# Kernel tuning notes

Hardware: AMD Instinct MI355X
Metric: run time of the kernel (lower is better)

Reference implementation:

```python
import jax, jax.numpy as jnp
import numpy as np

NA, NB = 50000, 10000        # node counts for types 'a' and 'b'
D_IN, D_OUT = 32, 64         # input feature dim, GRU hidden / GAT out dim
EA2A, EA2B, EB2A = 800000, 400000, 400000


def setup_inputs() -> dict:
    key = jax.random.key(0)
    ks = jax.random.split(key, 17)
    f32 = jnp.float32
    inp = {
        'x_a': jax.random.normal(ks[0], (NA, D_IN), f32),
        'x_b': jax.random.normal(ks[1], (NB, D_IN), f32),
        'h_a': jax.random.normal(ks[2], (NA, D_OUT), f32),
        'h_b': jax.random.normal(ks[3], (NB, D_OUT), f32),
        # stacked params: axis0 = gate (z,r,n); axis1 = node type (a,b) or edge type (a2a,a2b,b2a)
        'Wx': jax.random.normal(ks[4], (3, 2, D_IN, D_OUT), f32) * 0.05,
        'bx': jax.random.normal(ks[5], (3, 2, D_OUT), f32) * 0.05,
        'gat_ws': jax.random.normal(ks[6], (3, 3, D_OUT, D_OUT), f32) * 0.05,
        'gat_wd': jax.random.normal(ks[7], (3, 3, D_OUT, D_OUT), f32) * 0.05,
        'gat_as': jax.random.normal(ks[8], (3, 3, D_OUT), f32) * 0.05,
        'gat_ad': jax.random.normal(ks[9], (3, 3, D_OUT), f32) * 0.05,
        'gat_b': jax.random.normal(ks[10], (3, 3, D_OUT), f32) * 0.05,
        'ea2a_src': jax.random.randint(ks[11], (EA2A,), 0, NA, jnp.int32),
        'ea2a_dst': jax.random.randint(ks[12], (EA2A,), 0, NA, jnp.int32),
        'ea2b_src': jax.random.randint(ks[13], (EA2B,), 0, NA, jnp.int32),
        'ea2b_dst': jax.random.randint(ks[14], (EA2B,), 0, NB, jnp.int32),
        'eb2a_src': jax.random.randint(ks[15], (EB2A,), 0, NB, jnp.int32),
        'eb2a_dst': jax.random.randint(ks[16], (EB2A,), 0, NA, jnp.int32),
    }
    return inp


def _gat(hs, hd, src, dst, w_s, w_d, a_s, a_d, b, n_dst):
    """Single-head GATConv (PyG semantics, add_self_loops=False)."""
    xs = hs @ w_s                                   # [Ns, D] transformed sources
    xd = hd @ w_d                                   # [Nd, D] transformed destinations
    al_s = xs @ a_s                                 # [Ns]
    al_d = xd @ a_d                                 # [Nd]
    e = jax.nn.leaky_relu(al_s[src] + al_d[dst], 0.2)   # [E] raw attention logits
    m = jax.ops.segment_max(e, dst, num_segments=n_dst)
    m = jnp.where(jnp.isfinite(m), m, 0.0)          # empty segments -> 0 (unused)
    ex = jnp.exp(e - m[dst])
    denom = jax.ops.segment_sum(ex, dst, num_segments=n_dst)
    alpha = ex / (denom[dst] + 1e-16)               # segment softmax over in-edges
    out = jax.ops.segment_sum(alpha[:, None] * xs[src], dst, num_segments=n_dst)
    return out + b


def _hetero_conv(ha, hb, ws, wd, a_s, a_d, b, edges):
    """HeteroConv with sum aggregation across edge types per destination type."""
    (sa2a, da2a), (sa2b, da2b), (sb2a, db2a) = edges
    out_a = (_gat(ha, ha, sa2a, da2a, ws[0], wd[0], a_s[0], a_d[0], b[0], NA)
             + _gat(hb, ha, sb2a, db2a, ws[2], wd[2], a_s[2], a_d[2], b[2], NA))
    out_b = _gat(ha, hb, sa2b, da2b, ws[1], wd[1], a_s[1], a_d[1], b[1], NB)
    return out_a, out_b


def reference(x_a, x_b, h_a, h_b, Wx, bx, gat_ws, gat_wd, gat_as, gat_ad, gat_b,
              ea2a_src, ea2a_dst, ea2b_src, ea2b_dst, eb2a_src, eb2a_dst):
    edges = ((ea2a_src, ea2a_dst), (ea2b_src, ea2b_dst), (eb2a_src, eb2a_dst))

    def gate(g, ha_in, hb_in, act):
        ca, cb = _hetero_conv(ha_in, hb_in, gat_ws[g], gat_wd[g],
                              gat_as[g], gat_ad[g], gat_b[g], edges)
        ga = act(x_a @ Wx[g, 0] + ca + bx[g, 0])
        gb = act(x_b @ Wx[g, 1] + cb + bx[g, 1])
        return ga, gb

    z_a, z_b = gate(0, h_a, h_b, jax.nn.sigmoid)          # update gate
    r_a, r_b = gate(1, h_a, h_b, jax.nn.sigmoid)          # reset gate
    n_a, n_b = gate(2, r_a * h_a, r_b * h_b, jnp.tanh)    # candidate state
    new_a = (1.0 - z_a) * n_a + z_a * h_a
    new_b = (1.0 - z_b) * n_b + z_b * h_b
    return jnp.concatenate([new_a, new_b], axis=0)        # [NA+NB, D_OUT]
```

## Files before the change

### kernel.cpp

```cpp
#include <hip/hip_runtime.h>
#include <hip/hip_bf16.h>
#include <cstddef>
#include <cstdint>

#define NA 50000
#define NB 10000
#define D_IN 32
#define D_OUT 64
#define EA2A 800000
#define EA2B 400000
#define EB2A 400000
#define NCAT (NA + NB + NA)
#define ETOT (EA2A + EA2B + EB2A)
#define NCHUNK 8
#define CHUNK (NCAT / NCHUNK)
#define NSLICE 64
#define ESLICE (ETOT / NSLICE)

typedef unsigned int u32;
typedef unsigned short u16;
typedef __attribute__((ext_vector_type(8))) short short8_t;
typedef __attribute__((ext_vector_type(4))) float f32x4;
typedef __attribute__((ext_vector_type(2))) float f32x2;

__device__ __forceinline__ u32 bf16r(float x) {
    u32 u = __float_as_uint(x);
    u += 0x7fffu + ((u >> 16) & 1u);
    return u >> 16;
}
__device__ __forceinline__ float ubf(u32 bits) { return __uint_as_float(bits); }
__device__ __forceinline__ float sigm(float x) { return 1.f / (1.f + __expf(-x)); }
__device__ __forceinline__ u32 cvtpk(float lo, float hi) {
    u32 r;
    asm("v_cvt_pk_bf16_f32 %0, %1, %2" : "=v"(r) : "v"(lo), "v"(hi));
    return r;
}
__device__ __forceinline__ void pkfma(f32x2& acc, f32x2 x, f32x2 p) {
    asm("v_pk_fma_f32 %0, %1, %2, %0" : "+v"(acc) : "v"(x), "v"(p));
}

template <int CTRL, int RM>
__device__ __forceinline__ float dppf(float v) {
    return __int_as_float(__builtin_amdgcn_update_dpp(0, __float_as_int(v), CTRL, RM, 0xf, true));
}
__device__ __forceinline__ float wsum64(float v) {
    v += dppf<0x111, 0xf>(v);
    v += dppf<0x112, 0xf>(v);
    v += dppf<0x114, 0xf>(v);
    v += dppf<0x118, 0xf>(v);
    v += dppf<0x142, 0xa>(v);
    v += dppf<0x143, 0xc>(v);
    return __int_as_float(__builtin_amdgcn_readlane(__float_as_int(v), 63));
}

struct MmArgs {
    const float* H; int ntiles;
    const float* W0; const float* W1;
    void* XS; void* XS1;
    const float* SW[8]; const float* SA[8]; float* SOUT[8];
    int sstride; int nsc;
};

template <int NMAT, int PACKED>
__global__ void __launch_bounds__(256) gemm_mfma(MmArgs a)
{
    __shared__ float wvec[8][64];
    __shared__ short8_t bfr[NMAT * 8 + 2][64];
    int t = threadIdx.x;
    for (int idx = t; idx < a.nsc * 64; idx += 256) {
        int c = idx >> 6, k = idx & 63;
        const float* w = a.SW[c] + k * 64;
        const float* av = a.SA[c];
        float s = 0.f;
#pragma unroll 16
        for (int e = 0; e < 64; ++e) s = fmaf(w[e], av[e], s);
        wvec[c][k] = s;
    }
    __syncthreads();
    for (int idx = t; idx < NMAT * 8 * 64; idx += 256) {
        int fid = idx >> 6, l = idx & 63;
        int m = fid >> 3, r3 = fid & 7, tn = r3 >> 1, q = r3 & 1;
        const float* W = (NMAT == 2 && m == 1) ? a.W1 : a.W0;
        int kbase = 32 * q + ((l >> 4) << 3);
        int d = 16 * tn + (l & 15);
        short8_t v;
#pragma unroll
        for (int e = 0; e < 8; ++e) v[e] = (short)bf16r(W[(size_t)(kbase + e) * 64 + d]);
        bfr[fid][l] = v;
    }
    for (int idx = t; idx < 128; idx += 256) {
        int q = idx >> 6, l = idx & 63;
        int c = l & 15;
        int kbase = 32 * q + ((l >> 4) << 3);
        short8_t v;
#pragma unroll
        for (int e = 0; e < 8; ++e) v[e] = (c < a.nsc) ? (short)bf16r(wvec[c][kbase + e]) : (short)0;
        bfr[NMAT * 8 + q][l] = v;
    }
    __syncthreads();
    int lane = t & 63, wid = t >> 6;
    short8_t bw[NMAT][4][2], bs0, bs1;
#pragma unroll
    for (int m = 0; m < NMAT; ++m)
#pragma unroll
        for (int tn = 0; tn < 4; ++tn)
#pragma unroll
            for (int q = 0; q < 2; ++q) bw[m][tn][q] = bfr[m * 8 + tn * 2 + q][lane];
    bs0 = bfr[NMAT * 8][lane];
    bs1 = bfr[NMAT * 8 + 1][lane];

    int rl = lane & 15, kg = lane >> 4;
    f32x4 zero = {0.f, 0.f, 0.f, 0.f};
    for (int tile = blockIdx.x * 4 + wid; tile < a.ntiles; tile += gridDim.x * 4) {
        const float4* hp = (const float4*)(a.H + (size_t)(tile * 16 + rl) * 64) + kg * 2;
        float4 a0 = hp[0], a1 = hp[1];
        float4 b0 = hp[8], b1 = hp[9];
        union { short8_t s; u32 w[4]; } A0, A1;
        A0.w[0] = cvtpk(a0.x, a0.y); A0.w[1] = cvtpk(a0.z, a0.w);
        A0.w[2] = cvtpk(a1.x, a1.y); A0.w[3] = cvtpk(a1.z, a1.w);
        A1.w[0] = cvtpk(b0.x, b0.y); A1.w[1] = cvtpk(b0.z, b0.w);
        A1.w[2] = cvtpk(b1.x, b1.y); A1.w[3] = cvtpk(b1.z, b1.w);

        f32x4 acc[NMAT][4];
#pragma unroll
        for (int m = 0; m < NMAT; ++m)
#pragma unroll
            for (int tn = 0; tn < 4; ++tn) {
                f32x4 c0 = __builtin_amdgcn_mfma_f32_16x16x32_bf16(A0.s, bw[m][tn][0], zero, 0, 0, 0);
                acc[m][tn] = __builtin_amdgcn_mfma_f32_16x16x32_bf16(A1.s, bw[m][tn][1], c0, 0, 0, 0);
            }
        f32x4 accs = __builtin_amdgcn_mfma_f32_16x16x32_bf16(A0.s, bs0, zero, 0, 0, 0);
        accs = __builtin_amdgcn_mfma_f32_16x16x32_bf16(A1.s, bs1, accs, 0, 0, 0);

        int rbase = tile * 16 + kg * 4;
        if (NMAT == 2 && PACKED == 1) {
            u32* xo = (u32*)a.XS;
#pragma unroll
            for (int tn = 0; tn < 4; ++tn) {
                int d = tn * 16 + rl;
#pragma unroll
                for (int j = 0; j < 4; ++j)
                    xo[(size_t)(rbase + j) * 64 + d] = cvtpk(acc[0][tn][j], acc[1][tn][j]);
            }
        } else if (NMAT == 2 && PACKED == 0) {
            u16* xo0 = (u16*)a.XS;
            u16* xo1 = (u16*)a.XS1;
#pragma unroll
            for (int tn = 0; tn < 4; ++tn) {
                int d = tn * 16 + rl;
#pragma unroll
                for (int j = 0; j < 4; ++j) {
                    xo0[(size_t)(rbase + j) * 64 + d] = (u16)bf16r(acc[0][tn][j]);
                    xo1[(size_t)(rbase + j) * 64 + d] = (u16)bf16r(acc[1][tn][j]);
                }
            }
        } else {
            u16* xo = (u16*)a.XS;
#pragma unroll
            for (int tn = 0; tn < 4; ++tn) {
                int d = tn * 16 + rl;
#pragma unroll
                for (int j = 0; j < 4; ++j)
                    xo[(size_t)(rbase + j) * 64 + d] = (u16)bf16r(acc[0][tn][j]);
            }
        }
        if (rl < a.nsc) {
            float* so = a.SOUT[rl];
#pragma unroll
            for (int j = 0; j < 4; ++j) so[(size_t)(rbase + j) * a.sstride] = accs[j];
        }
    }
}

__global__ void __launch_bounds__(256) gemm_x_k(
    const float* __restrict__ xA, const float* __restrict__ xB,
    const float* __restrict__ Wx, const float* __restrict__ bx, const float* __restrict__ gb,
    u32* __restrict__ dzrA, u32* __restrict__ dzrB,
    u16* __restrict__ dnA, u16* __restrict__ dnB)
{
    __shared__ float Wsh[3 * 2048];
    __shared__ float cb[3 * 64];
    int t = threadIdx.x;
    int blk = blockIdx.x;
    bool isA = blk < (NA / 8);
    int ty = isA ? 0 : 1;
#pragma unroll
    for (int g = 0; g < 3; ++g) {
        const float4* s = (const float4*)(Wx + (size_t)(g * 2 + ty) * 2048);
        float4* d = (float4*)&Wsh[g * 2048];
        for (int i = t; i < 512; i += 256) d[i] = s[i];
    }
    if (t < 192) {
        int g = t >> 6, d = t & 63;
        float c = bx[(g * 2 + ty) * 64 + d];
        if (isA) c += gb[(g * 3 + 0) * 64 + d] + gb[(g * 3 + 2) * 64 + d];
        else     c += gb[(g * 3 + 1) * 64 + d];
        cb[t] = c;
    }
    __syncthreads();
    int lane = t & 63, wid = t >> 6;
    const float* X = isA ? xA : xB;
    int N = isA ? NA : NB;
    int rbase = (isA ? blk : blk - NA / 8) * 8 + wid * 2;
    float cz = cb[lane], cr = cb[64 + lane], cn = cb[128 + lane];
#pragma unroll
    for (int rr = 0; rr < 2; ++rr) {
        int r = rbase + rr;
        if (r >= N) break;
        float xv = (lane < 32) ? X[(size_t)r * 32 + lane] : 0.f;
        float az = cz, ar = cr, an = cn;
#pragma unroll
        for (int k = 0; k < 32; ++k) {
            float xk = __shfl(xv, k, 64);
            az = fmaf(xk, Wsh[k * 64 + lane], az);
            ar = fmaf(xk, Wsh[2048 + k * 64 + lane], ar);
            an = fmaf(xk, Wsh[4096 + k * 64 + lane], an);
        }
        u32 zr = bf16r(az) | (bf16r(ar) << 16);
        u16 nn = (u16)bf16r(an);
        if (isA) { dzrA[(size_t)r * 64 + lane] = zr; dnA[(size_t)r * 64 + lane] = nn; }
        else     { dzrB[(size_t)r * 64 + lane] = zr; dnB[(size_t)r * 64 + lane] = nn; }
    }
}

__global__ void __launch_bounds__(512) hist_k(
    const int* __restrict__ d0, const int* __restrict__ d1, const int* __restrict__ d2,
    u16* __restrict__ partial)
{
    __shared__ int hcnt[CHUNK];
    int k = blockIdx.x & (NCHUNK - 1);
    int s = blockIdx.x / NCHUNK;
    int lo = k * CHUNK;
    for (int i = threadIdx.x; i < CHUNK; i += 512) hcnt[i] = 0;
    __syncthreads();
    int e0 = s * ESLICE, e1 = e0 + ESLICE;
    for (int e = e0 + threadIdx.x; e < e1; e += 512) {
        int g;
        if (e < EA2A) g = d0[e];
        else if (e < EA2A + EA2B) g = NA + d1[e - EA2A];
        else g = NA + NB + d2[e - EA2A - EA2B];
        u32 rel = (u32)(g - lo);
        if (rel < CHUNK) atomicAdd(&hcnt[rel], 1);
    }
    __syncthreads();
    u16* po = partial + (size_t)s * NCAT + lo;
    for (int i = threadIdx.x; i < CHUNK; i += 512) po[i] = (u16)hcnt[i];
}

__global__ void scan_partial(const u16* __restrict__ partial, int* __restrict__ bsum, int N)
{
    __shared__ int sd[256];
    int t = threadIdx.x;
    int i = blockIdx.x * 256 + t;
    int v = 0;
    if (i < N) {
#pragma unroll 16
        for (int s = 0; s < NSLICE; ++s) v += partial[(size_t)s * NCAT + i];
    }
    sd[t] = v;
    __syncthreads();
    for (int off = 128; off; off >>= 1) {
        if (t < off) sd[t] += sd[t + off];
        __syncthreads();
    }
    if (t == 0) bsum[blockIdx.x] = sd[0];
}

__global__ void __launch_bounds__(512) scan_tops(int* bsum, int nb)
{
    __shared__ int sd[512];
    int t = threadIdx.x;
    int v = (t < nb) ? bsum[t] : 0;
    sd[t] = v;
    __syncthreads();
    for (int off = 1; off < 512; off <<= 1) {
        int add = (t >= off) ? sd[t - off] : 0;
        __syncthreads();
        sd[t] += add;
        __syncthreads();
    }
    if (t < nb) bsum[t] = sd[t] - v;
}

__global__ void scan_final(const u16* __restrict__ partial, const int* __restrict__ bsum,
                           int* __restrict__ rowptr, int* __restrict__ cnt,
                           u16* __restrict__ soff, int N)
{
    __shared__ int sd[256];
    int t = threadIdx.x;
    int i = blockIdx.x * 256 + t;
    int v = 0;
    if (i < N) {
#pragma unroll 16
        for (int s = 0; s < NSLICE; ++s) v += partial[(size_t)s * NCAT + i];
    }
    sd[t] = v;
    __syncthreads();
    for (int off = 1; off < 256; off <<= 1) {
        int add = (t >= off) ? sd[t - off] : 0;
        __syncthreads();
        sd[t] += add;
        __syncthreads();
    }
    if (i < N) {
        int rpi = bsum[blockIdx.x] + sd[t] - v;
        rowptr[i] = rpi;
        cnt[i] = v;
        int run = 0;
#pragma unroll 16
        for (int s = 0; s < NSLICE; ++s) {
            soff[(size_t)s * NCAT + i] = (u16)run;
            run += partial[(size_t)s * NCAT + i];
        }
    }
}

__global__ void __launch_bounds__(512) fill_k(
    const int* __restrict__ s0, const int* __restrict__ d0,
    const int* __restrict__ s1, const int* __restrict__ d1,
    const int* __restrict__ s2, const int* __restrict__ d2,
    const int* __restrict__ rp, const u16* __restrict__ soff, u16* __restrict__ csr)
{
    __shared__ int fpos[CHUNK];
    int k = blockIdx.x & (NCHUNK - 1);
    int s = blockIdx.x / NCHUNK;
    int lo = k * CHUNK;
    const u16* po = soff + (size_t)s * NCAT + lo;
    const int* rpo = rp + lo;
    for (int i = threadIdx.x; i < CHUNK; i += 512) fpos[i] = rpo[i] + (int)po[i];
    __syncthreads();
    int e0 = s * ESLICE, e1 = e0 + ESLICE;
    for (int e = e0 + threadIdx.x; e < e1; e += 512) {
        int g, sidx;
        const int* sp;
        if (e < EA2A) { g = d0[e]; sp = s0; sidx = e; }
        else if (e < EA2A + EA2B) { sidx = e - EA2A; g = NA + d1[sidx]; sp = s1; }
        else { sidx = e - EA2A - EA2B; g = NA + NB + d2[sidx]; sp = s2; }
        u32 rel = (u32)(g - lo);
        if (rel < CHUNK) {
            int src = sp[sidx];
            int p = atomicAdd(&fpos[rel], 1);
            csr[p] = (u16)src;
        }
    }
}

__device__ __forceinline__ void zr_pk(f32x2 azr[4], uint4 v, f32x2 p) {
    f32x2 x;
    x[0] = ubf(v.x << 16); x[1] = ubf(v.x & 0xffff0000u); pkfma(azr[0], x, p);
    x[0] = ubf(v.y << 16); x[1] = ubf(v.y & 0xffff0000u); pkfma(azr[1], x, p);
    x[0] = ubf(v.z << 16); x[1] = ubf(v.z & 0xffff0000u); pkfma(azr[2], x, p);
    x[0] = ubf(v.w << 16); x[1] = ubf(v.w & 0xffff0000u); pkfma(azr[3], x, p);
}

__device__ __forceinline__ void gat_zr_et(
    int gnode, int inode, int lane, int sub, int grp,
    const int* __restrict__ rp, const int* __restrict__ cnt, const u16* __restrict__ csr,
    const float2* __restrict__ als, const float2* __restrict__ ald,
    const uint4* __restrict__ xs,
    float oz[4], float orr[4])
{
    int deg = cnt[gnode];
    if (deg <= 0) return;
    int beg = rp[gnode];
    float2 ad = ald[inode];
    f32x2 azr[4];
#pragma unroll
    for (int q = 0; q < 4; ++q) { azr[q][0] = 0.f; azr[q][1] = 0.f; }
    float szl = 0.f, srl = 0.f;
    for (int base = 0; base < deg; base += 64) {
        int j = base + lane;
        int sj = 0; float pz = 0.f, pr = 0.f;
        if (j < deg) {
            sj = csr[beg + j];
            float2 al = als[sj];
            float tz = al.x + ad.x;
            float tr = al.y + ad.y;
            pz = __expf(fmaxf(tz, 0.2f * tz));
            pr = __expf(fmaxf(tr, 0.2f * tr));
        }
        szl += pz; srl += pr;
        u32 pk = (u32)sj | (bf16r(pz) << 16);
        int c = deg - base; if (c > 64) c = 64;
        int b = 0;
        for (; b + 16 <= c; b += 16) {
            u32 k0 = (u32)__shfl((int)pk, b + grp, 64);
            u32 k1 = (u32)__shfl((int)pk, b + 4 + grp, 64);
            u32 k2 = (u32)__shfl((int)pk, b + 8 + grp, 64);
            u32 k3 = (u32)__shfl((int)pk, b + 12 + grp, 64);
            float q0 = __shfl(pr, b + grp, 64);
            float q1 = __shfl(pr, b + 4 + grp, 64);
            float q2 = __shfl(pr, b + 8 + grp, 64);
            float q3 = __shfl(pr, b + 12 + grp, 64);
            uint4 v0 = xs[(size_t)(k0 & 0xffffu) * 16 + sub];
            uint4 v1 = xs[(size_t)(k1 & 0xffffu) * 16 + sub];
            uint4 v2 = xs[(size_t)(k2 & 0xffffu) * 16 + sub];
            uint4 v3 = xs[(size_t)(k3 & 0xffffu) * 16 + sub];
            f32x2 p;
            p[0] = ubf(k0 & 0xffff0000u); p[1] = q0; zr_pk(azr, v0, p);
            p[0] = ubf(k1 & 0xffff0000u); p[1] = q1; zr_pk(azr, v1, p);
            p[0] = ubf(k2 & 0xffff0000u); p[1] = q2; zr_pk(azr, v2, p);
            p[0] = ubf(k3 & 0xffff0000u); p[1] = q3; zr_pk(azr, v3, p);
        }
        for (; b < c; b += 4) {
            u32 k0 = (u32)__shfl((int)pk, b + grp, 64);
            float q0 = __shfl(pr, b + grp, 64);
            uint4 v0 = xs[(size_t)(k0 & 0xffffu) * 16 + sub];
            f32x2 p;
            p[0] = ubf(k0 & 0xffff0000u); p[1] = q0;
            zr_pk(azr, v0, p);
        }
    }
    float sz = wsum64(szl), sr = wsum64(srl);
    float rz = 1.f / (sz + 1e-16f), rr = 1.f / (sr + 1e-16f);
#pragma unroll
    for (int q = 0; q < 4; ++q) {
        oz[q] = fmaf(azr[q][0], rz, oz[q]);
        orr[q] = fmaf(azr[q][1], rr, orr[q]);
    }
}

__device__ __forceinline__ void n_pk4(f32x2 ac[4], uint4 v, f32x2 p) {
    f32x2 x;
    x[0] = ubf(v.x << 16); x[1] = ubf(v.x & 0xffff0000u); pkfma(ac[0], x, p);
    x[0] = ubf(v.y << 16); x[1] = ubf(v.y & 0xffff0000u); pkfma(ac[1], x, p);
    x[0] = ubf(v.z << 16); x[1] = ubf(v.z & 0xffff0000u); pkfma(ac[2], x, p);
    x[0] = ubf(v.w << 16); x[1] = ubf(v.w & 0xffff0000u); pkfma(ac[3], x, p);
}

__device__ __forceinline__ void gat_n_et(
    int gnode, int inode, int lane, int sub8, int grp8,
    const int* __restrict__ rp, const int* __restrict__ cnt, const u16* __restrict__ csr,
    const float* __restrict__ als, const float* __restrict__ ald,
    const uint4* __restrict__ xs,
    f32x2 oa[4])
{
    int deg = cnt[gnode];
    if (deg <= 0) return;
    int beg = rp[gnode];
    float ad = ald[inode];
    f32x2 ac[4];
#pragma unroll
    for (int q = 0; q < 4; ++q) { ac[q][0] = 0.f; ac[q][1] = 0.f; }
    float ssl = 0.f;
    for (int base = 0; base < deg; base += 64) {
        int j = base + lane;
        int sj = 0; float pv = 0.f;
        if (j < deg) {
            sj = csr[beg + j];
            float tv = als[sj] + ad;
            pv = __expf(fmaxf(tv, 0.2f * tv));
        }
        ssl += pv;
        u32 pk = (u32)sj | (bf16r(pv) << 16);
        int c = deg - base; if (c > 64) c = 64;
        int b = 0;
        for (; b + 32 <= c; b += 32) {
            u32 kk[4];
#pragma unroll
            for (int u = 0; u < 4; ++u) kk[u] = (u32)__shfl((int)pk, b + 8 * u + grp8, 64);
            uint4 vv[4];
#pragma unroll
            for (int u = 0; u < 4; ++u) vv[u] = xs[(size_t)(kk[u] & 0xffffu) * 8 + sub8];
#pragma unroll
            for (int u = 0; u < 4; ++u) {
                f32x2 p; p[0] = ubf(kk[u] & 0xffff0000u); p[1] = p[0];
                n_pk4(ac, vv[u], p);
            }
        }
        for (; b < c; b += 8) {
            u32 k0 = (u32)__shfl((int)pk, b + grp8, 64);
            uint4 v0 = xs[(size_t)(k0 & 0xffffu) * 8 + sub8];
            f32x2 p; p[0] = ubf(k0 & 0xffff0000u); p[1] = p[0];
            n_pk4(ac, v0, p);
        }
    }
    float ss = wsum64(ssl);
    float rs = 1.f / (ss + 1e-16f);
#pragma unroll
    for (int q = 0; q < 4; ++q) {
        oa[q][0] = fmaf(ac[q][0], rs, oa[q][0]);
        oa[q][1] = fmaf(ac[q][1], rs, oa[q][1]);
    }
}

struct ZrArgs {
    const int *rp, *cnt;
    const u16 *csr;
    const float2 *als0, *ald0, *als1, *ald1, *als2, *ald2;
    const uint4 *xs0, *xs1, *xs2;
    const u32 *dzrA, *dzrB;
    const float *hA, *hB;
    float *zA, *rhA, *zB, *rhB;
};

__global__ void __launch_bounds__(256) aggregate_zr_k(ZrArgs P)
{
    int t = threadIdx.x, lane = t & 63, wid = t >> 6;
    int sub = lane & 15, grp = lane >> 4;
    float oz[4] = {0.f, 0.f, 0.f, 0.f}, orr[4] = {0.f, 0.f, 0.f, 0.f};
    int blk = blockIdx.x;
    const u32* dzr; const float* Hp; float *Zp, *RHp;
    if (blk < NA / 4) {
        int i = blk * 4 + wid;
        gat_zr_et(i, i, lane, sub, grp, P.rp, P.cnt, P.csr, P.als0, P.ald0, P.xs0, oz, orr);
        gat_zr_et(NA + NB + i, i, lane, sub, grp, P.rp, P.cnt, P.csr, P.als2, P.ald2, P.xs2, oz, orr);
        dzr = P.dzrA + (size_t)i * 64; Hp = P.hA + (size_t)i * 64;
        Zp = P.zA + (size_t)i * 64; RHp = P.rhA + (size_t)i * 64;
    } else {
        int i = (blk - NA / 4) * 4 + wid;
        gat_zr_et(NA + i, i, lane, sub, grp, P.rp, P.cnt, P.csr, P.als1, P.ald1, P.xs1, oz, orr);
        dzr = P.dzrB + (size_t)i * 64; Hp = P.hB + (size_t)i * 64;
        Zp = P.zB + (size_t)i * 64; RHp = P.rhB + (size_t)i * 64;
    }
#pragma unroll
    for (int q = 0; q < 4; ++q) {
        oz[q] += __shfl_xor(oz[q], 16, 64); oz[q] += __shfl_xor(oz[q], 32, 64);
        orr[q] += __shfl_xor(orr[q], 16, 64); orr[q] += __shfl_xor(orr[q], 32, 64);
    }
    if (grp == 0) {
        uint4 d = *(const uint4*)(dzr + sub * 4);
        float4 h = *(const float4*)(Hp + sub * 4);
        float z0 = sigm(oz[0] + ubf(d.x << 16)), r0 = sigm(orr[0] + ubf(d.x & 0xffff0000u)) * h.x;
        float z1 = sigm(oz[1] + ubf(d.y << 16)), r1 = sigm(orr[1] + ubf(d.y & 0xffff0000u)) * h.y;
        float z2 = sigm(oz[2] + ubf(d.z << 16)), r2 = sigm(orr[2] + ubf(d.z & 0xffff0000u)) * h.z;
        float z3 = sigm(oz[3] + ubf(d.w << 16)), r3 = sigm(orr[3] + ubf(d.w & 0xffff0000u)) * h.w;
        *(float4*)(Zp + sub * 4) = make_float4(z0, z1, z2, z3);
        *(float4*)(RHp + sub * 4) = make_float4(r0, r1, r2, r3);
    }
}

struct NArgs {
    const int *rp, *cnt;
    const u16 *csr;
    const float *als0, *ald0, *als1, *ald1, *als2, *ald2;
    const uint4 *xs0, *xs1, *xs2;
    const u16 *dnA, *dnB;
    const float *hA, *hB, *zA, *zB;
    float *outA, *outB;
};

__global__ void __launch_bounds__(256) aggregate_n_k(NArgs P)
{
    int t = threadIdx.x, lane = t & 63, wid = t >> 6;
    int sub8 = lane & 7, grp8 = lane >> 3;
    f32x2 oa[4];
#pragma unroll
    for (int q = 0; q < 4; ++q) { oa[q][0] = 0.f; oa[q][1] = 0.f; }
    int blk = blockIdx.x;
    const u16* dn; const float *Hp, *Zp; float* Op;
    if (blk < NA / 4) {
        int i = blk * 4 + wid;
        gat_n_et(i, i, lane, sub8, grp8, P.rp, P.cnt, P.csr, P.als0, P.ald0, P.xs0, oa);
        gat_n_et(NA + NB + i, i, lane, sub8, grp8, P.rp, P.cnt, P.csr, P.als2, P.ald2, P.xs2, oa);
        dn = P.dnA + (size_t)i * 64; Hp = P.hA + (size_t)i * 64;
        Zp = P.zA + (size_t)i * 64; Op = P.outA + (size_t)i * 64;
    } else {
        int i = (blk - NA / 4) * 4 + wid;
        gat_n_et(NA + i, i, lane, sub8, grp8, P.rp, P.cnt, P.csr, P.als1, P.ald1, P.xs1, oa);
        dn = P.dnB + (size_t)i * 64; Hp = P.hB + (size_t)i * 64;
        Zp = P.zB + (size_t)i * 64; Op = P.outB + (size_t)i * 64;
    }
#pragma unroll
    for (int q = 0; q < 4; ++q) {
#pragma unroll
        for (int e = 0; e < 2; ++e) {
            oa[q][e] += __shfl_xor(oa[q][e], 8, 64);
            oa[q][e] += __shfl_xor(oa[q][e], 16, 64);
            oa[q][e] += __shfl_xor(oa[q][e], 32, 64);
        }
    }
    if (grp8 == 0) {
        uint4 d = *(const uint4*)(dn + sub8 * 8);
        float4 h0 = *(const float4*)(Hp + sub8 * 8);
        float4 h1 = *(const float4*)(Hp + sub8 * 8 + 4);
        float4 zv0 = *(const float4*)(Zp + sub8 * 8);
        float4 zv1 = *(const float4*)(Zp + sub8 * 8 + 4);
        float pre[8];
        pre[0] = oa[0][0] + ubf(d.x << 16); pre[1] = oa[0][1] + ubf(d.x & 0xffff0000u);
        pre[2] = oa[1][0] + ubf(d.y << 16); pre[3] = oa[1][1] + ubf(d.y & 0xffff0000u);
        pre[4] = oa[2][0] + ubf(d.z << 16); pre[5] = oa[2][1] + ubf(d.z & 0xffff0000u);
        pre[6] = oa[3][0] + ubf(d.w << 16); pre[7] = oa[3][1] + ubf(d.w & 0xffff0000u);
        float hh[8] = {h0.x, h0.y, h0.z, h0.w, h1.x, h1.y, h1.z, h1.w};
        float zz[8] = {zv0.x, zv0.y, zv0.z, zv0.w, zv1.x, zv1.y, zv1.z, zv1.w};
        float o[8];
#pragma unroll
        for (int q = 0; q < 8; ++q) {
            float x2 = fminf(fmaxf(pre[q] * 2.f, -30.f), 30.f);
            float ex = __expf(x2);
            float nv = (ex - 1.f) / (ex + 1.f);
            o[q] = (1.f - zz[q]) * nv + zz[q] * hh[q];
        }
        *(float4*)(Op + sub8 * 8) = make_float4(o[0], o[1], o[2], o[3]);
        *(float4*)(Op + sub8 * 8 + 4) = make_float4(o[4], o[5], o[6], o[7]);
    }
}

extern "C" void kernel_launch(void* const* d_in, const int* in_sizes, int n_in,
                              void* d_out, int out_size, void* d_ws, size_t ws_size,
                              hipStream_t stream)
{
    (void)in_sizes; (void)n_in; (void)out_size; (void)ws_size;
    const float* x_a = (const float*)d_in[0];
    const float* x_b = (const float*)d_in[1];
    const float* h_a = (const float*)d_in[2];
    const float* h_b = (const float*)d_in[3];
    const float* Wx  = (const float*)d_in[4];
    const float* bx  = (const float*)d_in[5];
    const float* gws = (const float*)d_in[6];
    const float* gwd = (const float*)d_in[7];
    const float* gas = (const float*)d_in[8];
    const float* gad = (const float*)d_in[9];
    const float* gb  = (const float*)d_in[10];
    const int* ea2a_s = (const int*)d_in[11];
    const int* ea2a_d = (const int*)d_in[12];
    const int* ea2b_s = (const int*)d_in[13];
    const int* ea2b_d = (const int*)d_in[14];
    const int* eb2a_s = (const int*)d_in[15];
    const int* eb2a_d = (const int*)d_in[16];
    float* out = (float*)d_out;

    char* w = (char*)d_ws;
    auto alloc = [&](size_t bytes) -> char* {
        char* p = w;
        w += (bytes + 255) & ~(size_t)255;
        return p;
    };
    char* xsblk = alloc((size_t)(NA + NA + NB) * 64 * 4);
    u32* xs_zr0 = (u32*)xsblk;
    u32* xs_zr1 = (u32*)(xsblk + (size_t)NA * 64 * 4);
    u32* xs_zr2 = (u32*)(xsblk + (size_t)(NA + NA) * 64 * 4);
    u16* xs_n0 = (u16*)xsblk;
    u16* xs_n1 = (u16*)(xsblk + (size_t)NA * 64 * 2);
    u16* xs_n2 = (u16*)(xsblk + (size_t)(NA + NA) * 64 * 2);
    char* alblk = alloc((size_t)(4 * NA + 2 * NB) * 2 * 4);
    float* als_zr0 = (float*)alblk;
    float* als_zr1 = als_zr0 + (size_t)NA * 2;
    float* als_zr2 = als_zr1 + (size_t)NA * 2;
    float* ald_zr0 = als_zr2 + (size_t)NB * 2;
    float* ald_zr1 = ald_zr0 + (size_t)NA * 2;
    float* ald_zr2 = ald_zr1 + (size_t)NB * 2;
    float* als_n0 = (float*)alblk;
    float* als_n1 = als_n0 + NA;
    float* als_n2 = als_n1 + NA;
    float* ald_n0 = als_n2 + NB;
    float* ald_n1 = ald_n0 + NA;
    float* ald_n2 = ald_n1 + NB;
    float* zbuf  = (float*)alloc((size_t)(NA + NB) * 64 * 4);
    float* rhbuf = (float*)alloc((size_t)(NA + NB) * 64 * 4);
    u32* dzrA = (u32*)alloc((size_t)NA * 64 * 4);
    u32* dzrB = (u32*)alloc((size_t)NB * 64 * 4);
    u16* dnA = (u16*)alloc((size_t)NA * 64 * 2);
    u16* dnB = (u16*)alloc((size_t)NB * 64 * 2);
    u16* partial = (u16*)alloc((size_t)NSLICE * NCAT * 2);
    u16* soff    = (u16*)alloc((size_t)NSLICE * NCAT * 2);
    int* cnt = (int*)alloc((size_t)NCAT * 4);
    int* rp  = (int*)alloc((size_t)NCAT * 4);
    u16* csr = (u16*)alloc((size_t)ETOT * 2);
    int* bsum = (int*)alloc(512 * 4);

    const int nbC = (NCAT + 255) / 256;

    hist_k<<<NCHUNK * NSLICE, 512, 0, stream>>>(ea2a_d, ea2b_d, eb2a_d, partial);
    scan_partial<<<nbC, 256, 0, stream>>>(partial, bsum, NCAT);
    scan_tops<<<1, 512, 0, stream>>>(bsum, nbC);
    scan_final<<<nbC, 256, 0, stream>>>(partial, bsum, rp, cnt, soff, NCAT);
    fill_k<<<NCHUNK * NSLICE, 512, 0, stream>>>(ea2a_s, ea2a_d, ea2b_s, ea2b_d, eb2a_s, eb2a_d,
                                                rp, soff, csr);

    gemm_x_k<<<(NA + NB) / 8, 256, 0, stream>>>(x_a, x_b, Wx, bx, gb, dzrA, dzrB, dnA, dnB);

    float* rh_a = rhbuf;
    float* rh_b = rhbuf + (size_t)NA * 64;
    float* z_a = zbuf;
    float* z_b = zbuf + (size_t)NA * 64;

    {
        MmArgs a{};
        a.H = h_a; a.ntiles = NA / 16;
        a.W0 = gws + 0 * 4096; a.W1 = gws + 3 * 4096;
        a.XS = xs_zr0;
        a.SW[0] = gws + 0 * 4096; a.SA[0] = gas + 0 * 64; a.SOUT[0] = als_zr0;
        a.SW[1] = gws + 3 * 4096; a.SA[1] = gas + 3 * 64; a.SOUT[1] = als_zr0 + 1;
        a.SW[2] = gws + 1 * 4096; a.SA[2] = gas + 1 * 64; a.SOUT[2] = als_zr1;
        a.SW[3] = gws + 4 * 4096; a.SA[3] = gas + 4 * 64; a.SOUT[3] = als_zr1 + 1;
        a.SW[4] = gwd + 0 * 4096; a.SA[4] = gad + 0 * 64; a.SOUT[4] = ald_zr0;
        a.SW[5] = gwd + 3 * 4096; a.SA[5] = gad + 3 * 64; a.SOUT[5] = ald_zr0 + 1;
        a.SW[6] = gwd + 2 * 4096; a.SA[6] = gad + 2 * 64; a.SOUT[6] = ald_zr2;
        a.SW[7] = gwd + 5 * 4096; a.SA[7] = gad + 5 * 64; a.SOUT[7] = ald_zr2 + 1;
        a.sstride = 2; a.nsc = 8;
        gemm_mfma<2, 1><<<320, 256, 0, stream>>>(a);
    }
    {
        MmArgs a{};
        a.H = h_a; a.ntiles = NA / 16;
        a.W0 = gws + 1 * 4096; a.W1 = gws + 4 * 4096;
        a.XS = xs_zr1;
        a.sstride = 1; a.nsc = 0;
        gemm_mfma<2, 1><<<320, 256, 0, stream>>>(a);
    }
    {
        MmArgs a{};
        a.H = h_b; a.ntiles = NB / 16;
        a.W0 = gws + 2 * 4096; a.W1 = gws + 5 * 4096;
        a.XS = xs_zr2;
        a.SW[0] = gws + 2 * 4096; a.SA[0] = gas + 2 * 64; a.SOUT[0] = als_zr2;
        a.SW[1] = gws + 5 * 4096; a.SA[1] = gas + 5 * 64; a.SOUT[1] = als_zr2 + 1;
        a.SW[2] = gwd + 1 * 4096; a.SA[2] = gad + 1 * 64; a.SOUT[2] = ald_zr1;
        a.SW[3] = gwd + 4 * 4096; a.SA[3] = gad + 4 * 64; a.SOUT[3] = ald_zr1 + 1;
        a.sstride = 2; a.nsc = 4;
        gemm_mfma<2, 1><<<80, 256, 0, stream>>>(a);
    }

    {
        ZrArgs P{};
        P.rp = rp; P.cnt = cnt; P.csr = csr;
        P.als0 = (const float2*)als_zr0; P.ald0 = (const float2*)ald_zr0;
        P.als1 = (const float2*)als_zr1; P.ald1 = (const float2*)ald_zr1;
        P.als2 = (const float2*)als_zr2; P.ald2 = (const float2*)ald_zr2;
        P.xs0 = (const uint4*)xs_zr0; P.xs1 = (const uint4*)xs_zr1; P.xs2 = (const uint4*)xs_zr2;
        P.dzrA = dzrA; P.dzrB = dzrB;
        P.hA = h_a; P.hB = h_b;
        P.zA = z_a; P.rhA = rh_a; P.zB = z_b; P.rhB = rh_b;
        aggregate_zr_k<<<(NA + NB) / 4, 256, 0, stream>>>(P);
    }

    {
        MmArgs a{};
        a.H = rh_a; a.ntiles = NA / 16;
        a.W0 = gws + 6 * 4096; a.W1 = gws + 7 * 4096;
        a.XS = xs_n0; a.XS1 = xs_n1;
        a.SW[0] = gws + 6 * 4096; a.SA[0] = gas + 6 * 64; a.SOUT[0] = als_n0;
        a.SW[1] = gws + 7 * 4096; a.SA[1] = gas + 7 * 64; a.SOUT[1] = als_n1;
        a.SW[2] = gwd + 6 * 4096; a.SA[2] = gad + 6 * 64; a.SOUT[2] = ald_n0;
        a.SW[3] = gwd + 8 * 4096; a.SA[3] = gad + 8 * 64; a.SOUT[3] = ald_n2;
        a.sstride = 1; a.nsc = 4;
        gemm_mfma<2, 0><<<320, 256, 0, stream>>>(a);
    }
    {
        MmArgs a{};
        a.H = rh_b; a.ntiles = NB / 16;
        a.W0 = gws + 8 * 4096; a.W1 = nullptr;
        a.XS = xs_n2;
        a.SW[0] = gws + 8 * 4096; a.SA[0] = gas + 8 * 64; a.SOUT[0] = als_n2;
        a.SW[1] = gwd + 7 * 4096; a.SA[1] = gad + 7 * 64; a.SOUT[1] = ald_n1;
        a.sstride = 1; a.nsc = 2;
        gemm_mfma<1, 1><<<80, 256, 0, stream>>>(a);
    }

    {
        NArgs P{};
        P.rp = rp; P.cnt = cnt; P.csr = csr;
        P.als0 = als_n0; P.ald0 = ald_n0;
        P.als1 = als_n1; P.ald1 = ald_n1;
        P.als2 = als_n2; P.ald2 = ald_n2;
        P.xs0 = (const uint4*)xs_n0; P.xs1 = (const uint4*)xs_n1; P.xs2 = (const uint4*)xs_n2;
        P.dnA = dnA; P.dnB = dnB;
        P.hA = h_a; P.hB = h_b; P.zA = z_a; P.zB = z_b;
        P.outA = out; P.outB = out + (size_t)NA * 64;
        aggregate_n_k<<<(NA + NB) / 4, 256, 0, stream>>>(P);
    }
}
```

Baseline: 316.5 us.

## Batch MFMA GEMM launches, store r*h as bf16, fold top-level scan into final scan

The three z/r projection GEMMs and the two candidate-gate GEMMs each become a single launch, with each block choosing its sub-problem from the block index. The r*h intermediate is now written as packed bf16 and read directly by the GEMM, which halves that buffer's traffic and drops the in-kernel conversion. The separate scan_tops kernel is removed: each scan_final block reduces the preceding block sums itself. gemm_x_k uses a fixed grid with a grid-stride loop. In exchange, the type-b candidate GEMM now computes a redundant second matrix into a scratch buffer, and scan_final repeats the prefix-sum reduction in every block.

Result: no change. 314.9 us (-0.5%).

```diff
diff --git a/kernel.cpp b/kernel.cpp
--- a/kernel.cpp
+++ b/kernel.cpp
@@ -54,18 +54,28 @@
 }
 
 struct MmArgs {
-    const float* H; int ntiles;
+    const void* H; int ntiles;
     const float* W0; const float* W1;
     void* XS; void* XS1;
     const float* SW[8]; const float* SA[8]; float* SOUT[8];
     int sstride; int nsc;
 };
-
-template <int NMAT, int PACKED>
-__global__ void __launch_bounds__(256) gemm_mfma(MmArgs a)
+struct MmMulti {
+    MmArgs r[3];
+    int n0, n1;
+};
+
+template <int NMAT, int PACKED, int HB16>
+__global__ void __launch_bounds__(256) gemm_mfma(MmMulti m)
 {
     __shared__ float wvec[8][64];
     __shared__ short8_t bfr[NMAT * 8 + 2][64];
+    int b = blockIdx.x;
+    const MmArgs* Rp; int lb, nb;
+    if (b < m.n0) { Rp = &m.r[0]; lb = b; nb = m.n0; }
+    else if (b < m.n0 + m.n1) { Rp = &m.r[1]; lb = b - m.n0; nb = m.n1; }
+    else { Rp = &m.r[2]; lb = b - m.n0 - m.n1; nb = gridDim.x - m.n0 - m.n1; }
+    const MmArgs a = *Rp;
     int t = threadIdx.x;
     for (int idx = t; idx < a.nsc * 64; idx += 256) {
         int c = idx >> 6, k = idx & 63;
@@ -79,8 +89,8 @@
     __syncthreads();
     for (int idx = t; idx < NMAT * 8 * 64; idx += 256) {
         int fid = idx >> 6, l = idx & 63;
-        int m = fid >> 3, r3 = fid & 7, tn = r3 >> 1, q = r3 & 1;
-        const float* W = (NMAT == 2 && m == 1) ? a.W1 : a.W0;
+        int mm = fid >> 3, r3 = fid & 7, tn = r3 >> 1, q = r3 & 1;
+        const float* W = (NMAT == 2 && mm == 1) ? a.W1 : a.W0;
         int kbase = 32 * q + ((l >> 4) << 3);
         int d = 16 * tn + (l & 15);
         short8_t v;
@@ -101,33 +111,39 @@
     int lane = t & 63, wid = t >> 6;
     short8_t bw[NMAT][4][2], bs0, bs1;
 #pragma unroll
-    for (int m = 0; m < NMAT; ++m)
+    for (int mm = 0; mm < NMAT; ++mm)
 #pragma unroll
         for (int tn = 0; tn < 4; ++tn)
 #pragma unroll
-            for (int q = 0; q < 2; ++q) bw[m][tn][q] = bfr[m * 8 + tn * 2 + q][lane];
+            for (int q = 0; q < 2; ++q) bw[mm][tn][q] = bfr[mm * 8 + tn * 2 + q][lane];
     bs0 = bfr[NMAT * 8][lane];
     bs1 = bfr[NMAT * 8 + 1][lane];
 
     int rl = lane & 15, kg = lane >> 4;
     f32x4 zero = {0.f, 0.f, 0.f, 0.f};
-    for (int tile = blockIdx.x * 4 + wid; tile < a.ntiles; tile += gridDim.x * 4) {
-        const float4* hp = (const float4*)(a.H + (size_t)(tile * 16 + rl) * 64) + kg * 2;
-        float4 a0 = hp[0], a1 = hp[1];
-        float4 b0 = hp[8], b1 = hp[9];
-        union { short8_t s; u32 w[4]; } A0, A1;
-        A0.w[0] = cvtpk(a0.x, a0.y); A0.w[1] = cvtpk(a0.z, a0.w);
-        A0.w[2] = cvtpk(a1.x, a1.y); A0.w[3] = cvtpk(a1.z, a1.w);
-        A1.w[0] = cvtpk(b0.x, b0.y); A1.w[1] = cvtpk(b0.z, b0.w);
-        A1.w[2] = cvtpk(b1.x, b1.y); A1.w[3] = cvtpk(b1.z, b1.w);
+    for (int tile = lb * 4 + wid; tile < a.ntiles; tile += nb * 4) {
+        union { uint4 u; short8_t s; } A0, A1;
+        if (HB16) {
+            const uint4* hp = (const uint4*)((const u16*)a.H + (size_t)(tile * 16 + rl) * 64);
+            A0.u = hp[kg];
+            A1.u = hp[4 + kg];
+        } else {
+            const float4* hp = (const float4*)((const float*)a.H + (size_t)(tile * 16 + rl) * 64) + kg * 2;
+            float4 a0 = hp[0], a1 = hp[1];
+            float4 b0 = hp[8], b1 = hp[9];
+            A0.u.x = cvtpk(a0.x, a0.y); A0.u.y = cvtpk(a0.z, a0.w);
+            A0.u.z = cvtpk(a1.x, a1.y); A0.u.w = cvtpk(a1.z, a1.w);
+            A1.u.x = cvtpk(b0.x, b0.y); A1.u.y = cvtpk(b0.z, b0.w);
+            A1.u.z = cvtpk(b1.x, b1.y); A1.u.w = cvtpk(b1.z, b1.w);
+        }
 
         f32x4 acc[NMAT][4];
 #pragma unroll
-        for (int m = 0; m < NMAT; ++m)
+        for (int mm = 0; mm < NMAT; ++mm)
 #pragma unroll
             for (int tn = 0; tn < 4; ++tn) {
-                f32x4 c0 = __builtin_amdgcn_mfma_f32_16x16x32_bf16(A0.s, bw[m][tn][0], zero, 0, 0, 0);
-                acc[m][tn] = __builtin_amdgcn_mfma_f32_16x16x32_bf16(A1.s, bw[m][tn][1], c0, 0, 0, 0);
+                f32x4 c0 = __builtin_amdgcn_mfma_f32_16x16x32_bf16(A0.s, bw[mm][tn][0], zero, 0, 0, 0);
+                acc[mm][tn] = __builtin_amdgcn_mfma_f32_16x16x32_bf16(A1.s, bw[mm][tn][1], c0, 0, 0, 0);
             }
         f32x4 accs = __builtin_amdgcn_mfma_f32_16x16x32_bf16(A0.s, bs0, zero, 0, 0, 0);
         accs = __builtin_amdgcn_mfma_f32_16x16x32_bf16(A1.s, bs1, accs, 0, 0, 0);
@@ -182,7 +198,7 @@
     __shared__ float cb[3 * 64];
     int t = threadIdx.x;
     int blk = blockIdx.x;
-    bool isA = blk < (NA / 8);
+    bool isA = blk < 448;
     int ty = isA ? 0 : 1;
 #pragma unroll
     for (int g = 0; g < 3; ++g) {
@@ -201,25 +217,28 @@
     int lane = t & 63, wid = t >> 6;
     const float* X = isA ? xA : xB;
     int N = isA ? NA : NB;
-    int rbase = (isA ? blk : blk - NA / 8) * 8 + wid * 2;
+    int nblk = isA ? 448 : 64;
+    int lb = isA ? blk : blk - 448;
     float cz = cb[lane], cr = cb[64 + lane], cn = cb[128 + lane];
-#pragma unroll
-    for (int rr = 0; rr < 2; ++rr) {
-        int r = rbase + rr;
-        if (r >= N) break;
-        float xv = (lane < 32) ? X[(size_t)r * 32 + lane] : 0.f;
-        float az = cz, ar = cr, an = cn;
-#pragma unroll
-        for (int k = 0; k < 32; ++k) {
-            float xk = __shfl(xv, k, 64);
-            az = fmaf(xk, Wsh[k * 64 + lane], az);
-            ar = fmaf(xk, Wsh[2048 + k * 64 + lane], ar);
-            an = fmaf(xk, Wsh[4096 + k * 64 + lane], an);
-        }
-        u32 zr = bf16r(az) | (bf16r(ar) << 16);
-        u16 nn = (u16)bf16r(an);
-        if (isA) { dzrA[(size_t)r * 64 + lane] = zr; dnA[(size_t)r * 64 + lane] = nn; }
-        else     { dzrB[(size_t)r * 64 + lane] = zr; dnB[(size_t)r * 64 + lane] = nn; }
+    for (int r0 = (lb * 4 + wid) * 2; r0 < N; r0 += nblk * 8) {
+#pragma unroll
+        for (int rr = 0; rr < 2; ++rr) {
+            int r = r0 + rr;
+            if (r >= N) break;
+            float xv = (lane < 32) ? X[(size_t)r * 32 + lane] : 0.f;
+            float az = cz, ar = cr, an = cn;
+#pragma unroll
+            for (int k = 0; k < 32; ++k) {
+                float xk = __shfl(xv, k, 64);
+                az = fmaf(xk, Wsh[k * 64 + lane], az);
+                ar = fmaf(xk, Wsh[2048 + k * 64 + lane], ar);
+                an = fmaf(xk, Wsh[4096 + k * 64 + lane], an);
+            }
+            u32 zr = bf16r(az) | (bf16r(ar) << 16);
+            u16 nn = (u16)bf16r(an);
+            if (isA) { dzrA[(size_t)r * 64 + lane] = zr; dnA[(size_t)r * 64 + lane] = nn; }
+            else     { dzrB[(size_t)r * 64 + lane] = zr; dnB[(size_t)r * 64 + lane] = nn; }
+        }
     }
 }
 
@@ -266,28 +285,23 @@
     if (t == 0) bsum[blockIdx.x] = sd[0];
 }
 
-__global__ void __launch_bounds__(512) scan_tops(int* bsum, int nb)
-{
-    __shared__ int sd[512];
-    int t = threadIdx.x;
-    int v = (t < nb) ? bsum[t] : 0;
-    sd[t] = v;
-    __syncthreads();
-    for (int off = 1; off < 512; off <<= 1) {
-        int add = (t >= off) ? sd[t - off] : 0;
-        __syncthreads();
-        sd[t] += add;
-        __syncthreads();
-    }
-    if (t < nb) bsum[t] = sd[t] - v;
-}
-
 __global__ void scan_final(const u16* __restrict__ partial, const int* __restrict__ bsum,
                            int* __restrict__ rowptr, int* __restrict__ cnt,
                            u16* __restrict__ soff, int N)
 {
     __shared__ int sd[256];
+    __shared__ int rbuf[256];
     int t = threadIdx.x;
+    int acc = 0;
+    for (int j = t; j < blockIdx.x; j += 256) acc += bsum[j];
+    rbuf[t] = acc;
+    __syncthreads();
+    for (int off = 128; off; off >>= 1) {
+        if (t < off) rbuf[t] += rbuf[t + off];
+        __syncthreads();
+    }
+    int base = rbuf[0];
+    __syncthreads();
     int i = blockIdx.x * 256 + t;
     int v = 0;
     if (i < N) {
@@ -303,7 +317,7 @@
         __syncthreads();
     }
     if (i < N) {
-        int rpi = bsum[blockIdx.x] + sd[t] - v;
+        int rpi = base + sd[t] - v;
         rowptr[i] = rpi;
         cnt[i] = v;
         int run = 0;
@@ -491,7 +505,8 @@
     const uint4 *xs0, *xs1, *xs2;
     const u32 *dzrA, *dzrB;
     const float *hA, *hB;
-    float *zA, *rhA, *zB, *rhB;
+    float *zA, *zB;
+    u16 *rhA, *rhB;
 };
 
 __global__ void __launch_bounds__(256) aggregate_zr_k(ZrArgs P)
@@ -500,7 +515,7 @@
     int sub = lane & 15, grp = lane >> 4;
     float oz[4] = {0.f, 0.f, 0.f, 0.f}, orr[4] = {0.f, 0.f, 0.f, 0.f};
     int blk = blockIdx.x;
-    const u32* dzr; const float* Hp; float *Zp, *RHp;
+    const u32* dzr; const float* Hp; float* Zp; u16* RHp;
     if (blk < NA / 4) {
         int i = blk * 4 + wid;
         gat_zr_et(i, i, lane, sub, grp, P.rp, P.cnt, P.csr, P.als0, P.ald0, P.xs0, oz, orr);
@@ -526,7 +541,10 @@
         float z2 = sigm(oz[2] + ubf(d.z << 16)), r2 = sigm(orr[2] + ubf(d.z & 0xffff0000u)) * h.z;
         float z3 = sigm(oz[3] + ubf(d.w << 16)), r3 = sigm(orr[3] + ubf(d.w & 0xffff0000u)) * h.w;
         *(float4*)(Zp + sub * 4) = make_float4(z0, z1, z2, z3);
-        *(float4*)(RHp + sub * 4) = make_float4(r0, r1, r2, r3);
+        uint2 rhp;
+        rhp.x = cvtpk(r0, r1);
+        rhp.y = cvtpk(r2, r3);
+        *(uint2*)(RHp + sub * 4) = rhp;
     }
 }
 
@@ -647,7 +665,7 @@
     float* ald_n1 = ald_n0 + NA;
     float* ald_n2 = ald_n1 + NB;
     float* zbuf  = (float*)alloc((size_t)(NA + NB) * 64 * 4);
-    float* rhbuf = (float*)alloc((size_t)(NA + NB) * 64 * 4);
+    u16* rhbuf = (u16*)alloc((size_t)(NA + NB) * 64 * 2);
     u32* dzrA = (u32*)alloc((size_t)NA * 64 * 4);
     u32* dzrB = (u32*)alloc((size_t)NB * 64 * 4);
     u16* dnA = (u16*)alloc((size_t)NA * 64 * 2);
@@ -658,58 +676,51 @@
     int* rp  = (int*)alloc((size_t)NCAT * 4);
     u16* csr = (u16*)alloc((size_t)ETOT * 2);
     int* bsum = (int*)alloc(512 * 4);
+    u16* nscr = (u16*)alloc((size_t)NB * 64 * 2);
 
     const int nbC = (NCAT + 255) / 256;
 
     hist_k<<<NCHUNK * NSLICE, 512, 0, stream>>>(ea2a_d, ea2b_d, eb2a_d, partial);
     scan_partial<<<nbC, 256, 0, stream>>>(partial, bsum, NCAT);
-    scan_tops<<<1, 512, 0, stream>>>(bsum, nbC);
     scan_final<<<nbC, 256, 0, stream>>>(partial, bsum, rp, cnt, soff, NCAT);
     fill_k<<<NCHUNK * NSLICE, 512, 0, stream>>>(ea2a_s, ea2a_d, ea2b_s, ea2b_d, eb2a_s, eb2a_d,
                                                 rp, soff, csr);
 
-    gemm_x_k<<<(NA + NB) / 8, 256, 0, stream>>>(x_a, x_b, Wx, bx, gb, dzrA, dzrB, dnA, dnB);
-
-    float* rh_a = rhbuf;
-    float* rh_b = rhbuf + (size_t)NA * 64;
+    gemm_x_k<<<512, 256, 0, stream>>>(x_a, x_b, Wx, bx, gb, dzrA, dzrB, dnA, dnB);
+
+    u16* rh_a = rhbuf;
+    u16* rh_b = rhbuf + (size_t)NA * 64;
     float* z_a = zbuf;
     float* z_b = zbuf + (size_t)NA * 64;
 
     {
-        MmArgs a{};
-        a.H = h_a; a.ntiles = NA / 16;
-        a.W0 = gws + 0 * 4096; a.W1 = gws + 3 * 4096;
-        a.XS = xs_zr0;
-        a.SW[0] = gws + 0 * 4096; a.SA[0] = gas + 0 * 64; a.SOUT[0] = als_zr0;
-        a.SW[1] = gws + 3 * 4096; a.SA[1] = gas + 3 * 64; a.SOUT[1] = als_zr0 + 1;
-        a.SW[2] = gws + 1 * 4096; a.SA[2] = gas + 1 * 64; a.SOUT[2] = als_zr1;
-        a.SW[3] = gws + 4 * 4096; a.SA[3] = gas + 4 * 64; a.SOUT[3] = als_zr1 + 1;
-        a.SW[4] = gwd + 0 * 4096; a.SA[4] = gad + 0 * 64; a.SOUT[4] = ald_zr0;
-        a.SW[5] = gwd + 3 * 4096; a.SA[5] = gad + 3 * 64; a.SOUT[5] = ald_zr0 + 1;
-        a.SW[6] = gwd + 2 * 4096; a.SA[6] = gad + 2 * 64; a.SOUT[6] = ald_zr2;
-        a.SW[7] = gwd + 5 * 4096; a.SA[7] = gad + 5 * 64; a.SOUT[7] = ald_zr2 + 1;
-        a.sstride = 2; a.nsc = 8;
-        gemm_mfma<2, 1><<<320, 256, 0, stream>>>(a);
-    }
-    {
-        MmArgs a{};
-        a.H = h_a; a.ntiles = NA / 16;
-        a.W0 = gws + 1 * 4096; a.W1 = gws + 4 * 4096;
-        a.XS = xs_zr1;
-        a.sstride = 1; a.nsc = 0;
-        gemm_mfma<2, 1><<<320, 256, 0, stream>>>(a);
-    }
-    {
-        MmArgs a{};
-        a.H = h_b; a.ntiles = NB / 16;
-        a.W0 = gws + 2 * 4096; a.W1 = gws + 5 * 4096;
-        a.XS = xs_zr2;
-        a.SW[0] = gws + 2 * 4096; a.SA[0] = gas + 2 * 64; a.SOUT[0] = als_zr2;
-        a.SW[1] = gws + 5 * 4096; a.SA[1] = gas + 5 * 64; a.SOUT[1] = als_zr2 + 1;
-        a.SW[2] = gwd + 1 * 4096; a.SA[2] = gad + 1 * 64; a.SOUT[2] = ald_zr1;
-        a.SW[3] = gwd + 4 * 4096; a.SA[3] = gad + 4 * 64; a.SOUT[3] = ald_zr1 + 1;
-        a.sstride = 2; a.nsc = 4;
-        gemm_mfma<2, 1><<<80, 256, 0, stream>>>(a);
+        MmMulti M{};
+        M.n0 = 320; M.n1 = 320;
+        M.r[0].H = h_a; M.r[0].ntiles = NA / 16;
+        M.r[0].W0 = gws + 0 * 4096; M.r[0].W1 = gws + 3 * 4096;
+        M.r[0].XS = xs_zr0;
+        M.r[0].SW[0] = gws + 0 * 4096; M.r[0].SA[0] = gas + 0 * 64; M.r[0].SOUT[0] = als_zr0;
+        M.r[0].SW[1] = gws + 3 * 4096; M.r[0].SA[1] = gas + 3 * 64; M.r[0].SOUT[1] = als_zr0 + 1;
+        M.r[0].SW[2] = gws + 1 * 4096; M.r[0].SA[2] = gas + 1 * 64; M.r[0].SOUT[2] = als_zr1;
+        M.r[0].SW[3] = gws + 4 * 4096; M.r[0].SA[3] = gas + 4 * 64; M.r[0].SOUT[3] = als_zr1 + 1;
+        M.r[0].SW[4] = gwd + 0 * 4096; M.r[0].SA[4] = gad + 0 * 64; M.r[0].SOUT[4] = ald_zr0;
+        M.r[0].SW[5] = gwd + 3 * 4096; M.r[0].SA[5] = gad + 3 * 64; M.r[0].SOUT[5] = ald_zr0 + 1;
+        M.r[0].SW[6] = gwd + 2 * 4096; M.r[0].SA[6] = gad + 2 * 64; M.r[0].SOUT[6] = ald_zr2;
+        M.r[0].SW[7] = gwd + 5 * 4096; M.r[0].SA[7] = gad + 5 * 64; M.r[0].SOUT[7] = ald_zr2 + 1;
+        M.r[0].sstride = 2; M.r[0].nsc = 8;
+        M.r[1].H = h_a; M.r[1].ntiles = NA / 16;
+        M.r[1].W0 = gws + 1 * 4096; M.r[1].W1 = gws + 4 * 4096;
+        M.r[1].XS = xs_zr1;
+        M.r[1].sstride = 1; M.r[1].nsc = 0;
+        M.r[2].H = h_b; M.r[2].ntiles = NB / 16;
+        M.r[2].W0 = gws + 2 * 4096; M.r[2].W1 = gws + 5 * 4096;
+        M.r[2].XS = xs_zr2;
+        M.r[2].SW[0] = gws + 2 * 4096; M.r[2].SA[0] = gas + 2 * 64; M.r[2].SOUT[0] = als_zr2;
+        M.r[2].SW[1] = gws + 5 * 4096; M.r[2].SA[1] = gas + 5 * 64; M.r[2].SOUT[1] = als_zr2 + 1;
+        M.r[2].SW[2] = gwd + 1 * 4096; M.r[2].SA[2] = gad + 1 * 64; M.r[2].SOUT[2] = ald_zr1;
+        M.r[2].SW[3] = gwd + 4 * 4096; M.r[2].SA[3] = gad + 4 * 64; M.r[2].SOUT[3] = ald_zr1 + 1;
+        M.r[2].sstride = 2; M.r[2].nsc = 4;
+        gemm_mfma<2, 1, 0><<<720, 256, 0, stream>>>(M);
     }
 
     {
@@ -721,31 +732,28 @@
         P.xs0 = (const uint4*)xs_zr0; P.xs1 = (const uint4*)xs_zr1; P.xs2 = (const uint4*)xs_zr2;
         P.dzrA = dzrA; P.dzrB = dzrB;
         P.hA = h_a; P.hB = h_b;
-        P.zA = z_a; P.rhA = rh_a; P.zB = z_b; P.rhB = rh_b;
+        P.zA = z_a; P.zB = z_b; P.rhA = rh_a; P.rhB = rh_b;
         aggregate_zr_k<<<(NA + NB) / 4, 256, 0, stream>>>(P);
     }
 
     {
-        MmArgs a{};
-        a.H = rh_a; a.ntiles = NA / 16;
-        a.W0 = gws + 6 * 4096; a.W1 = gws + 7 * 4096;
-        a.XS = xs_n0; a.XS1 = xs_n1;
-        a.SW[0] = gws + 6 * 4096; a.SA[0] = gas + 6 * 64; a.SOUT[0] = als_n0;
-        a.SW[1] = gws + 7 * 4096; a.SA[1] = gas + 7 * 64; a.SOUT[1] = als_n1;
-        a.SW[2] = gwd + 6 * 4096; a.SA[2] = gad + 6 * 64; a.SOUT[2] = ald_n0;
-        a.SW[3] = gwd + 8 * 4096; a.SA[3] = gad + 8 * 64; a.SOUT[3] = ald_n2;
-        a.sstride = 1; a.nsc = 4;
-        gemm_mfma<2, 0><<<320, 256, 0, stream>>>(a);
-    }
-    {
-        MmArgs a{};
-        a.H = rh_b; a.ntiles = NB / 16;
-        a.W0 = gws + 8 * 4096; a.W1 = nullptr;
-        a.XS = xs_n2;
-        a.SW[0] = gws + 8 * 4096; a.SA[0] = gas + 8 * 64; a.SOUT[0] = als_n2;
-        a.SW[1] = gwd + 7 * 4096; a.SA[1] = gad + 7 * 64; a.SOUT[1] = ald_n1;
-        a.sstride = 1; a.nsc = 2;
-        gemm_mfma<1, 1><<<80, 256, 0, stream>>>(a);
+        MmMulti M{};
+        M.n0 = 320; M.n1 = 80;
+        M.r[0].H = rh_a; M.r[0].ntiles = NA / 16;
+        M.r[0].W0 = gws + 6 * 4096; M.r[0].W1 = gws + 7 * 4096;
+        M.r[0].XS = xs_n0; M.r[0].XS1 = xs_n1;
+        M.r[0].SW[0] = gws + 6 * 4096; M.r[0].SA[0] = gas + 6 * 64; M.r[0].SOUT[0] = als_n0;
+        M.r[0].SW[1] = gws + 7 * 4096; M.r[0].SA[1] = gas + 7 * 64; M.r[0].SOUT[1] = als_n1;
+        M.r[0].SW[2] = gwd + 6 * 4096; M.r[0].SA[2] = gad + 6 * 64; M.r[0].SOUT[2] = ald_n0;
+        M.r[0].SW[3] = gwd + 8 * 4096; M.r[0].SA[3] = gad + 8 * 64; M.r[0].SOUT[3] = ald_n2;
+        M.r[0].sstride = 1; M.r[0].nsc = 4;
+        M.r[1].H = rh_b; M.r[1].ntiles = NB / 16;
+        M.r[1].W0 = gws + 8 * 4096; M.r[1].W1 = gws + 8 * 4096;
+        M.r[1].XS = xs_n2; M.r[1].XS1 = nscr;
+        M.r[1].SW[0] = gws + 8 * 4096; M.r[1].SA[0] = gas + 8 * 64; M.r[1].SOUT[0] = als_n2;
+        M.r[1].SW[1] = gwd + 7 * 4096; M.r[1].SA[1] = gad + 7 * 64; M.r[1].SOUT[1] = ald_n1;
+        M.r[1].sstride = 1; M.r[1].nsc = 2;
+        gemm_mfma<2, 0, 1><<<400, 256, 0, stream>>>(M);
     }
 
     {
```
